# Performance work log

Measured on AMD Instinct MI355X. Metric: run time of the kernel, lower is better.

Reference implementation:

```python
import jax, jax.numpy as jnp
import numpy as np

D_IN = 1024
D_OUT = 1024
B = 4
S = 2048


def setup_inputs() -> dict:
    key = jax.random.key(0)
    kx, kq, kk, kv = jax.random.split(key, 4)
    x = jax.random.normal(kx, (B, S, D_IN), dtype=jnp.float32)
    # Linear weights stored as [d_in, d_out] so projection is x @ W
    sc = 1.0 / np.sqrt(D_IN)
    Wq = jax.random.normal(kq, (D_IN, D_OUT), dtype=jnp.float32) * sc
    Wk = jax.random.normal(kk, (D_IN, D_OUT), dtype=jnp.float32) * sc
    Wv = jax.random.normal(kv, (D_IN, D_OUT), dtype=jnp.float32) * sc
    return {"x": x, "Wq": Wq, "Wk": Wk, "Wv": Wv}


def reference(x, Wq, Wk, Wv):
    # q, k, v: [b, s, d_out]
    q = jnp.einsum("bsd,de->bse", x, Wq)
    k = jnp.einsum("bsd,de->bse", x, Wk)
    v = jnp.einsum("bsd,de->bse", x, Wv)
    s = q.shape[1]
    # raw scores [b, s, s]
    scores = jnp.einsum("bqd,bkd->bqk", q, k)
    # causal mask: disallow key j > query i (see notes re: original mask bug)
    causal = jnp.triu(jnp.ones((s, s), dtype=bool), k=1)
    scores = jnp.where(causal[None, :, :], -jnp.inf, scores)
    scale = 1.0 / jnp.sqrt(jnp.asarray(k.shape[-1], dtype=scores.dtype))
    att_weights = jax.nn.softmax(scores * scale, axis=-1)
    # dropout p=0.0 -> identity
    att_output = jnp.einsum("bqk,bkd->bqd", att_weights, v)
    return att_output, att_weights
```

## Files before the change

### kernel.cpp

```cpp
#include <hip/hip_runtime.h>
#include <stdint.h>

#define DIM 1024
#define SEQ 2048
#define NB 4

typedef unsigned short u16;
typedef __bf16 bf16x8 __attribute__((ext_vector_type(8)));
typedef float floatx4 __attribute__((ext_vector_type(4)));

__device__ __forceinline__ u16 f32_to_bf16(float f) {
  union { float f; unsigned u; } v; v.f = f;
  unsigned r = v.u + 0x7FFFu + ((v.u >> 16) & 1u);
  return (u16)(r >> 16);
}

__device__ __forceinline__ void async16(const void* g, void* l) {
  __builtin_amdgcn_global_load_lds(
      (__attribute__((address_space(1))) unsigned int*)g,
      (__attribute__((address_space(3))) unsigned int*)l, 16, 0, 0);
}

__global__ __launch_bounds__(256) void k_prep(const float* __restrict__ x,
                                              const float* __restrict__ Wq,
                                              const float* __restrict__ Wk,
                                              const float* __restrict__ Wv,
                                              u16* __restrict__ xb,
                                              u16* __restrict__ wt) {
  __shared__ u16 tile[32][33];
  const int bid = blockIdx.x;
  const int tid = threadIdx.x;
  if (bid < 4096) {
    int i = bid * 256 + tid;
    float4 a = ((const float4*)x)[i * 2];
    float4 b = ((const float4*)x)[i * 2 + 1];
    ushort4 o0, o1;
    o0.x = f32_to_bf16(a.x); o0.y = f32_to_bf16(a.y);
    o0.z = f32_to_bf16(a.z); o0.w = f32_to_bf16(a.w);
    o1.x = f32_to_bf16(b.x); o1.y = f32_to_bf16(b.y);
    o1.z = f32_to_bf16(b.z); o1.w = f32_to_bf16(b.w);
    ((ushort4*)xb)[i * 2] = o0;
    ((ushort4*)xb)[i * 2 + 1] = o1;
  } else {
    int t = bid - 4096;
    int z = t >> 10;
    int ti = t & 1023;
    int c0 = (ti & 31) * 32, r0 = (ti >> 5) * 32;
    const float* src = (z == 0) ? Wq : (z == 1) ? Wk : Wv;
    u16* d = wt + (size_t)z * DIM * DIM;
    int tx = tid & 31, ty = tid >> 5;
    #pragma unroll
    for (int dy = 0; dy < 32; dy += 8)
      tile[ty + dy][tx] = f32_to_bf16(src[(size_t)(r0 + ty + dy) * DIM + c0 + tx]);
    __syncthreads();
    #pragma unroll
    for (int dy = 0; dy < 32; dy += 8)
      d[(size_t)(c0 + ty + dy) * DIM + r0 + tx] = tile[tx][ty + dy];
  }
}


#define STG(PG, STBASE, SLOT, H, I, KT)                                        \
  async16((PG) + (size_t)((H) * 128 + (I) * 64) * DIM + (KT) * 64,             \
          (STBASE) + (SLOT) * 16384 + (H) * 8192 + (I) * 4096)

#define PHASE(SLOT, KS, MH, RDB, STAGE, SYNC)                                  \
  {                                                                            \
    const int go_ = (KS) ? ga1 : ga0;                                          \
    const u16* pa_ = aRd + (SLOT) * 16384;                                     \
    if (RDB) {                                                                 \
      const u16* pb_ = bRd + (SLOT) * 16384;                                   \
      _Pragma("unroll") for (int n = 0; n < 4; ++n)                            \
          bfr[n] = *(const bf16x8*)(pb_ + n * 1024 + go_);                     \
    }                                                                          \
    _Pragma("unroll") for (int m = 0; m < 4; ++m)                              \
        af[m] = *(const bf16x8*)(pa_ + ((MH) * 4 + m) * 1024 + go_);           \
    STAGE                                                                      \
    __builtin_amdgcn_s_barrier();                                              \
    asm volatile("s_waitcnt lgkmcnt(0)" ::: "memory");                         \
    __builtin_amdgcn_sched_barrier(0);                                         \
    __builtin_amdgcn_s_setprio(1);                                             \
    _Pragma("unroll") for (int m = 0; m < 4; ++m)                              \
        _Pragma("unroll") for (int n = 0; n < 4; ++n)                          \
            acc[(MH) * 4 + m][n] = __builtin_amdgcn_mfma_f32_16x16x32_bf16(    \
                af[m], bfr[n], acc[(MH) * 4 + m][n], 0, 0, 0);                 \
    __builtin_amdgcn_s_setprio(0);                                             \
    SYNC                                                                       \
    __builtin_amdgcn_s_barrier();                                              \
  }

__global__ __launch_bounds__(512) void k_proj8(const u16* __restrict__ xb,
                                               const u16* __restrict__ wt,
                                               u16* __restrict__ qk,
                                               u16* __restrict__ vT) {
  __shared__ u16 lds[65536];
  const int wg = ((blockIdx.x & 7) * 48) + (blockIdx.x >> 3);
  const int tid = threadIdx.x;
  const int lane = tid & 63;
  const int wid = tid >> 6;

  const u16 *A, *Bt;
  u16* Cout;
  int ldc;
  if (wg < 256) {
    const int z = wg >> 7;
    const int r = wg & 127;
    const int mt = r >> 2, nt = r & 3;
    A = xb + (size_t)mt * 256 * DIM;
    Bt = wt + (size_t)z * DIM * DIM + (size_t)nt * 256 * DIM;
    Cout = qk + (size_t)z * (NB * SEQ * DIM) + (size_t)mt * 256 * DIM + nt * 256;
    ldc = DIM;
  } else {
    const int r = wg - 256;
    const int mt = r >> 5, nt = r & 31;
    A = wt + (size_t)2 * DIM * DIM + (size_t)mt * 256 * DIM;
    Bt = xb + (size_t)nt * 256 * DIM;
    Cout = vT + (size_t)(nt >> 3) * (DIM * SEQ) + (size_t)mt * 256 * SEQ
              + (nt & 7) * 256;
    ldc = SEQ;
  }

  const int srow = wid * 8 + (lane >> 3);
  const int gsrc = (lane & 7) ^ ((lane >> 3) & 7);
  const u16* pga = A + (size_t)srow * DIM + gsrc * 8;
  const u16* pgb = Bt + (size_t)srow * DIM + gsrc * 8;
  u16* stA = lds + wid * 512;
  u16* stB = lds + 32768 + wid * 512;

  const int wr = wid >> 2, wc = wid & 3;
  const int lrow = lane & 15, quad = lane >> 4;
  const int s = lrow & 7;
  const u16* aRd = lds + (wr * 128 + lrow) * 64;
  const u16* bRd = lds + 32768 + (wc * 64 + lrow) * 64;
  const int ga0 = (quad ^ s) << 3;
  const int ga1 = ga0 ^ 32;

  floatx4 acc[8][4] = {};
  bf16x8 af[4], bfr[4];

  STG(pga, stA, 0, 0, 0, 0); STG(pga, stA, 0, 0, 1, 0);
  STG(pga, stA, 0, 1, 0, 0); STG(pga, stA, 0, 1, 1, 0);
  STG(pgb, stB, 0, 0, 0, 0); STG(pgb, stB, 0, 0, 1, 0);
  STG(pgb, stB, 0, 1, 0, 0); STG(pgb, stB, 0, 1, 1, 0);
  STG(pgb, stB, 1, 0, 0, 1); STG(pgb, stB, 1, 0, 1, 1);
  asm volatile("s_waitcnt vmcnt(2)" ::: "memory");
  __builtin_amdgcn_s_barrier();

  const int NITER = DIM / 128;
  for (int t = 0; t < NITER; ++t) {
    const bool more = (t + 1 < NITER);
    const int kA1 = 2 * t + 1;
    const int kN = 2 * t + 2;
    const int kB1n = 2 * t + 3;

    PHASE(0, 0, 0, 1,
          { STG(pga, stA, 1, 0, 0, kA1); STG(pga, stA, 1, 0, 1, kA1); }, {})
    PHASE(0, 0, 1, 0,
          { STG(pga, stA, 1, 1, 0, kA1); STG(pga, stA, 1, 1, 1, kA1); }, {})
    PHASE(0, 1, 0, 1,
          { STG(pgb, stB, 1, 1, 0, kA1); STG(pgb, stB, 1, 1, 1, kA1); }, {})
    PHASE(0, 1, 1, 0,
          { if (more) { STG(pgb, stB, 0, 0, 0, kN); STG(pgb, stB, 0, 0, 1, kN); } },
          { if (more) asm volatile("s_waitcnt vmcnt(2)" ::: "memory");
            else      asm volatile("s_waitcnt vmcnt(0)" ::: "memory"); })
    PHASE(1, 0, 0, 1,
          { if (more) { STG(pgb, stB, 0, 1, 0, kN); STG(pgb, stB, 0, 1, 1, kN); } }, {})
    PHASE(1, 0, 1, 0,
          { if (more) { STG(pga, stA, 0, 0, 0, kN); STG(pga, stA, 0, 0, 1, kN); } }, {})
    PHASE(1, 1, 0, 1,
          { if (more) { STG(pga, stA, 0, 1, 0, kN); STG(pga, stA, 0, 1, 1, kN); } }, {})
    PHASE(1, 1, 1, 0,
          { if (more) { STG(pgb, stB, 1, 0, 0, kB1n); STG(pgb, stB, 1, 0, 1, kB1n); } },
          { if (more) asm volatile("s_waitcnt vmcnt(2)" ::: "memory"); })
  }

  asm volatile("s_waitcnt vmcnt(0)" ::: "memory");

  u16* C = Cout + (size_t)(wr * 128 + quad * 4) * ldc + wc * 64 + lrow;
  #pragma unroll
  for (int m = 0; m < 8; ++m)
    #pragma unroll
    for (int rr = 0; rr < 4; ++rr)
      #pragma unroll
      for (int n = 0; n < 4; ++n)
        C[(size_t)(m * 16 + rr) * ldc + n * 16] = f32_to_bf16(acc[m][n][rr]);
}

__device__ __forceinline__ void mfma_core128(const u16* __restrict__ A, int lda,
                                             const u16* __restrict__ Bt, int ldb,
                                             int kchunks, u16* lds,
                                             floatx4 acc[4][4]) {
  const int tid = threadIdx.x;
  const int lane = tid & 63;
  const int wid = tid >> 6;
  u16* lds_a = lds;
  u16* lds_b = lds + 16384;

  const int srow4 = lane >> 4;
  const int sgr = lane & 15;
  const int gbase = sgr ^ srow4;
  const u16* ag0 = A + (size_t)(wid * 32 + srow4) * lda + gbase * 8;
  const u16* ag1 = A + (size_t)(wid * 32 + srow4) * lda + (gbase ^ 4) * 8;
  const u16* bg0 = Bt + (size_t)(wid * 32 + srow4) * ldb + gbase * 8;
  const u16* bg1 = Bt + (size_t)(wid * 32 + srow4) * ldb + (gbase ^ 4) * 8;
  u16* la = lds_a + wid * 4096;
  u16* lb = lds_b + wid * 4096;

  const int wm = (wid >> 1) * 64, wn = (wid & 1) * 64;
  const int lrow = lane & 15, quad = lane >> 4;
  const int s = lrow & 7;
  const u16* pa = lds_a + (wm + lrow) * 128;
  const u16* pb = lds_b + (wn + lrow) * 128;

  for (int kt = 0; kt < kchunks; ++kt) {
    #pragma unroll
    for (int c = 0; c < 8; ++c) {
      const u16* sa = ((c & 1) ? ag1 : ag0) + (size_t)(c * 4) * lda;
      async16(sa, la + c * 512);
    }
    #pragma unroll
    for (int c = 0; c < 8; ++c) {
      const u16* sb = ((c & 1) ? bg1 : bg0) + (size_t)(c * 4) * ldb;
      async16(sb, lb + c * 512);
    }
    ag0 += 128; ag1 += 128; bg0 += 128; bg1 += 128;
    __syncthreads();
    #pragma unroll
    for (int ks = 0; ks < 4; ++ks) {
      const int g = (((ks << 2) | quad) ^ s) << 3;
      bf16x8 af[4], bfr[4];
      #pragma unroll
      for (int t = 0; t < 4; ++t) af[t] = *(const bf16x8*)(pa + t * 2048 + g);
      #pragma unroll
      for (int t = 0; t < 4; ++t) bfr[t] = *(const bf16x8*)(pb + t * 2048 + g);
      #pragma unroll
      for (int i = 0; i < 4; ++i)
        #pragma unroll
        for (int j = 0; j < 4; ++j)
          acc[i][j] = __builtin_amdgcn_mfma_f32_16x16x32_bf16(af[i], bfr[j],
                                                              acc[i][j], 0, 0, 0);
    }
    __syncthreads();
  }
}

__global__ __launch_bounds__(256) void k_scores(const u16* __restrict__ q,
                                                const u16* __restrict__ k,
                                                float* __restrict__ w) {
  const int id = blockIdx.x;
  const int b = id & 3;
  int t = id >> 2;
  int mt = (int)((sqrtf(8.0f * (float)t + 1.0f) - 1.0f) * 0.5f);
  while ((mt + 1) * (mt + 2) / 2 <= t) ++mt;
  while (mt * (mt + 1) / 2 > t) --mt;
  const int nt = t - mt * (mt + 1) / 2;
  __shared__ u16 lds[32768];
  floatx4 acc[4][4] = {};
  mfma_core128(q + (size_t)b * SEQ * DIM + (size_t)mt * 128 * DIM, DIM,
               k + (size_t)b * SEQ * DIM + (size_t)nt * 128 * DIM, DIM,
               DIM / 128, lds, acc);
  const int lane = threadIdx.x & 63, wid = threadIdx.x >> 6;
  const int wm = (wid >> 1) * 64, wn = (wid & 1) * 64;
  const int lrow = lane & 15, quad = lane >> 4;
  float* C = w + (size_t)b * SEQ * SEQ
               + (size_t)(mt * 128 + wm + quad * 4) * SEQ + nt * 128 + wn + lrow;
  #pragma unroll
  for (int i = 0; i < 4; ++i)
    #pragma unroll
    for (int rr = 0; rr < 4; ++rr)
      #pragma unroll
      for (int j = 0; j < 4; ++j)
        C[(size_t)(i * 16 + rr) * SEQ + j * 16] = acc[i][j][rr] * 0.03125f;
}

__global__ __launch_bounds__(256) void k_softmax(float* __restrict__ w,
                                                 u16* __restrict__ P) {
  const int r = blockIdx.x;
  const int i = r & (SEQ - 1);
  const int len = i + 1;
  const int plen4 = (((i >> 7) + 1) << 7) >> 2;
  float4* srow = (float4*)(w + (size_t)r * SEQ);
  ushort4* prow = (ushort4*)(P + (size_t)r * SEQ);
  const int tid = threadIdx.x;
  const int lane = tid & 63, wid = tid >> 6;
  __shared__ float rm[4], rs[4];

  float4 e[2];
  float mx = -1e30f;
  #pragma unroll
  for (int u = 0; u < 2; ++u) {
    int q4 = tid + u * 256;
    int j0 = q4 * 4;
    float4 v = make_float4(-1e30f, -1e30f, -1e30f, -1e30f);
    if (j0 < len) {
      v = srow[q4];
      v.x = (j0 + 0 < len) ? v.x : -1e30f;
      v.y = (j0 + 1 < len) ? v.y : -1e30f;
      v.z = (j0 + 2 < len) ? v.z : -1e30f;
      v.w = (j0 + 3 < len) ? v.w : -1e30f;
    }
    e[u] = v;
    mx = fmaxf(mx, fmaxf(fmaxf(v.x, v.y), fmaxf(v.z, v.w)));
  }
  #pragma unroll
  for (int o = 32; o >= 1; o >>= 1) mx = fmaxf(mx, __shfl_xor(mx, o, 64));
  if (lane == 0) rm[wid] = mx;
  __syncthreads();
  mx = fmaxf(fmaxf(rm[0], rm[1]), fmaxf(rm[2], rm[3]));

  float sum = 0.f;
  #pragma unroll
  for (int u = 0; u < 2; ++u) {
    e[u].x = __expf(e[u].x - mx);
    e[u].y = __expf(e[u].y - mx);
    e[u].z = __expf(e[u].z - mx);
    e[u].w = __expf(e[u].w - mx);
    sum += e[u].x + e[u].y + e[u].z + e[u].w;
  }
  #pragma unroll
  for (int o = 32; o >= 1; o >>= 1) sum += __shfl_xor(sum, o, 64);
  if (lane == 0) rs[wid] = sum;
  __syncthreads();
  sum = rs[0] + rs[1] + rs[2] + rs[3];
  const float inv = 1.0f / sum;

  #pragma unroll
  for (int u = 0; u < 2; ++u) {
    int q4 = tid + u * 256;
    int j0 = q4 * 4;
    float4 v;
    v.x = (j0 + 0 < len) ? e[u].x * inv : 0.f;
    v.y = (j0 + 1 < len) ? e[u].y * inv : 0.f;
    v.z = (j0 + 2 < len) ? e[u].z * inv : 0.f;
    v.w = (j0 + 3 < len) ? e[u].w * inv : 0.f;
    srow[q4] = v;
    if (q4 < plen4) {
      ushort4 p;
      p.x = f32_to_bf16(v.x); p.y = f32_to_bf16(v.y);
      p.z = f32_to_bf16(v.z); p.w = f32_to_bf16(v.w);
      prow[q4] = p;
    }
  }
}

__global__ __launch_bounds__(256) void k_pv(const u16* __restrict__ P,
                                            const u16* __restrict__ vT,
                                            float* __restrict__ out) {
  const int id = blockIdx.x;
  const int mt = 15 - (id >> 5);
  const int nt = (id >> 2) & 7;
  const int b = id & 3;
  __shared__ u16 lds[32768];
  floatx4 acc[4][4] = {};
  mfma_core128(P + (size_t)b * SEQ * SEQ + (size_t)mt * 128 * SEQ, SEQ,
               vT + (size_t)b * DIM * SEQ + (size_t)nt * 128 * SEQ, SEQ,
               mt + 1, lds, acc);
  const int lane = threadIdx.x & 63, wid = threadIdx.x >> 6;
  const int wm = (wid >> 1) * 64, wn = (wid & 1) * 64;
  const int lrow = lane & 15, quad = lane >> 4;
  float* C = out + (size_t)b * SEQ * DIM
                 + (size_t)(mt * 128 + wm + quad * 4) * DIM + nt * 128 + wn + lrow;
  #pragma unroll
  for (int i = 0; i < 4; ++i)
    #pragma unroll
    for (int rr = 0; rr < 4; ++rr)
      #pragma unroll
      for (int j = 0; j < 4; ++j)
        C[(size_t)(i * 16 + rr) * DIM + j * 16] = acc[i][j][rr];
}

extern "C" void kernel_launch(void* const* d_in, const int* in_sizes, int n_in,
                              void* d_out, int out_size, void* d_ws, size_t ws_size,
                              hipStream_t stream) {
  const float* x  = (const float*)d_in[0];
  const float* Wq = (const float*)d_in[1];
  const float* Wk = (const float*)d_in[2];
  const float* Wv = (const float*)d_in[3];
  float* att_out = (float*)d_out;
  float* att_w   = (float*)d_out + 8388608;

  u16* xb = (u16*)d_ws;
  u16* wt = xb + 8388608;
  u16* qk = wt + 3145728;
  u16* vT = qk + 16777216;
  u16* P  = vT + 8388608;

  k_prep<<<7168, 256, 0, stream>>>(x, Wq, Wk, Wv, xb, wt);
  k_proj8<<<384, 512, 0, stream>>>(xb, wt, qk, vT);
  k_scores<<<544, 256, 0, stream>>>(qk, qk + 8388608, att_w);
  k_softmax<<<8192, 256, 0, stream>>>(att_w, P);
  k_pv<<<512, 256, 0, stream>>>(P, vT, att_out);
}
```

Before: 269.0 us.

## Double-buffer LDS fragment registers so MFMAs overlap next phase's LDS reads

```diff
diff --git a/kernel.cpp b/kernel.cpp
--- a/kernel.cpp
+++ b/kernel.cpp
@@ -64,27 +64,38 @@
   async16((PG) + (size_t)((H) * 128 + (I) * 64) * DIM + (KT) * 64,             \
           (STBASE) + (SLOT) * 16384 + (H) * 8192 + (I) * 4096)
 
-#define PHASE(SLOT, KS, MH, RDB, STAGE, SYNC)                                  \
+#define LOADAF(AF, SLOT, KS, MH)                                               \
+  { const u16* pa_ = aRd + (SLOT) * 16384;                                     \
+    const int g_ = (KS) ? ga1 : ga0;                                           \
+    AF[0] = *(const bf16x8*)(pa_ + ((MH) * 4 + 0) * 1024 + g_);                \
+    AF[1] = *(const bf16x8*)(pa_ + ((MH) * 4 + 1) * 1024 + g_);                \
+    AF[2] = *(const bf16x8*)(pa_ + ((MH) * 4 + 2) * 1024 + g_);                \
+    AF[3] = *(const bf16x8*)(pa_ + ((MH) * 4 + 3) * 1024 + g_); }
+
+#define LOADBF(BF, SLOT, KS)                                                   \
+  { const u16* pb_ = bRd + (SLOT) * 16384;                                     \
+    const int g_ = (KS) ? ga1 : ga0;                                           \
+    BF[0] = *(const bf16x8*)(pb_ + 0 * 1024 + g_);                             \
+    BF[1] = *(const bf16x8*)(pb_ + 1 * 1024 + g_);                             \
+    BF[2] = *(const bf16x8*)(pb_ + 2 * 1024 + g_);                             \
+    BF[3] = *(const bf16x8*)(pb_ + 3 * 1024 + g_); }
+
+#define MFMA16(AFU, BFU, MH)                                                   \
+  _Pragma("unroll") for (int m_ = 0; m_ < 4; ++m_)                             \
+      _Pragma("unroll") for (int n_ = 0; n_ < 4; ++n_)                         \
+          acc[(MH) * 4 + m_][n_] = __builtin_amdgcn_mfma_f32_16x16x32_bf16(    \
+              AFU[m_], BFU[n_], acc[(MH) * 4 + m_][n_], 0, 0, 0);
+
+#define PH(AFU, BFU, MH, PRELOAD, STGS, SYNC)                                  \
   {                                                                            \
-    const int go_ = (KS) ? ga1 : ga0;                                          \
-    const u16* pa_ = aRd + (SLOT) * 16384;                                     \
-    if (RDB) {                                                                 \
-      const u16* pb_ = bRd + (SLOT) * 16384;                                   \
-      _Pragma("unroll") for (int n = 0; n < 4; ++n)                            \
-          bfr[n] = *(const bf16x8*)(pb_ + n * 1024 + go_);                     \
-    }                                                                          \
-    _Pragma("unroll") for (int m = 0; m < 4; ++m)                              \
-        af[m] = *(const bf16x8*)(pa_ + ((MH) * 4 + m) * 1024 + go_);           \
-    STAGE                                                                      \
+    PRELOAD                                                                    \
+    STGS                                                                       \
     __builtin_amdgcn_s_barrier();                                              \
+    __builtin_amdgcn_s_setprio(1);                                             \
+    MFMA16(AFU, BFU, MH);                                                      \
+    __builtin_amdgcn_s_setprio(0);                                             \
     asm volatile("s_waitcnt lgkmcnt(0)" ::: "memory");                         \
     __builtin_amdgcn_sched_barrier(0);                                         \
-    __builtin_amdgcn_s_setprio(1);                                             \
-    _Pragma("unroll") for (int m = 0; m < 4; ++m)                              \
-        _Pragma("unroll") for (int n = 0; n < 4; ++n)                          \
-            acc[(MH) * 4 + m][n] = __builtin_amdgcn_mfma_f32_16x16x32_bf16(    \
-                af[m], bfr[n], acc[(MH) * 4 + m][n], 0, 0, 0);                 \
-    __builtin_amdgcn_s_setprio(0);                                             \
     SYNC                                                                       \
     __builtin_amdgcn_s_barrier();                                              \
   }
@@ -136,15 +147,20 @@
   const int ga1 = ga0 ^ 32;
 
   floatx4 acc[8][4] = {};
-  bf16x8 af[4], bfr[4];
+  bf16x8 afA[4], afB[4], bfrP[4], bfrQ[4];
 
   STG(pga, stA, 0, 0, 0, 0); STG(pga, stA, 0, 0, 1, 0);
   STG(pga, stA, 0, 1, 0, 0); STG(pga, stA, 0, 1, 1, 0);
   STG(pgb, stB, 0, 0, 0, 0); STG(pgb, stB, 0, 0, 1, 0);
   STG(pgb, stB, 0, 1, 0, 0); STG(pgb, stB, 0, 1, 1, 0);
   STG(pgb, stB, 1, 0, 0, 1); STG(pgb, stB, 1, 0, 1, 1);
-  asm volatile("s_waitcnt vmcnt(2)" ::: "memory");
+  STG(pgb, stB, 1, 1, 0, 1); STG(pgb, stB, 1, 1, 1, 1);
+  asm volatile("s_waitcnt vmcnt(4)" ::: "memory");
   __builtin_amdgcn_s_barrier();
+  LOADAF(afA, 0, 0, 0);
+  LOADBF(bfrP, 0, 0);
+  asm volatile("s_waitcnt lgkmcnt(0)" ::: "memory");
+  __builtin_amdgcn_sched_barrier(0);
 
   const int NITER = DIM / 128;
   for (int t = 0; t < NITER; ++t) {
@@ -153,25 +169,33 @@
     const int kN = 2 * t + 2;
     const int kB1n = 2 * t + 3;
 
-    PHASE(0, 0, 0, 1,
-          { STG(pga, stA, 1, 0, 0, kA1); STG(pga, stA, 1, 0, 1, kA1); }, {})
-    PHASE(0, 0, 1, 0,
-          { STG(pga, stA, 1, 1, 0, kA1); STG(pga, stA, 1, 1, 1, kA1); }, {})
-    PHASE(0, 1, 0, 1,
-          { STG(pgb, stB, 1, 1, 0, kA1); STG(pgb, stB, 1, 1, 1, kA1); }, {})
-    PHASE(0, 1, 1, 0,
-          { if (more) { STG(pgb, stB, 0, 0, 0, kN); STG(pgb, stB, 0, 0, 1, kN); } },
-          { if (more) asm volatile("s_waitcnt vmcnt(2)" ::: "memory");
-            else      asm volatile("s_waitcnt vmcnt(0)" ::: "memory"); })
-    PHASE(1, 0, 0, 1,
-          { if (more) { STG(pgb, stB, 0, 1, 0, kN); STG(pgb, stB, 0, 1, 1, kN); } }, {})
-    PHASE(1, 0, 1, 0,
-          { if (more) { STG(pga, stA, 0, 0, 0, kN); STG(pga, stA, 0, 0, 1, kN); } }, {})
-    PHASE(1, 1, 0, 1,
-          { if (more) { STG(pga, stA, 0, 1, 0, kN); STG(pga, stA, 0, 1, 1, kN); } }, {})
-    PHASE(1, 1, 1, 0,
-          { if (more) { STG(pgb, stB, 1, 0, 0, kB1n); STG(pgb, stB, 1, 0, 1, kB1n); } },
-          { if (more) asm volatile("s_waitcnt vmcnt(2)" ::: "memory"); })
+    PH(afA, bfrP, 0,
+       LOADAF(afB, 0, 0, 1);,
+       STG(pga, stA, 1, 0, 0, kA1); STG(pga, stA, 1, 0, 1, kA1);, {})
+    PH(afB, bfrP, 1,
+       LOADAF(afA, 0, 1, 0); LOADBF(bfrQ, 0, 1);,
+       STG(pga, stA, 1, 1, 0, kA1); STG(pga, stA, 1, 1, 1, kA1);, {})
+    PH(afA, bfrQ, 0,
+       LOADAF(afB, 0, 1, 1);,
+       if (more) { STG(pgb, stB, 0, 0, 0, kN); STG(pgb, stB, 0, 0, 1, kN); },
+       if (more) { asm volatile("s_waitcnt vmcnt(2)" ::: "memory"); }
+       else      { asm volatile("s_waitcnt vmcnt(0)" ::: "memory"); })
+    PH(afB, bfrQ, 1,
+       LOADAF(afA, 1, 0, 0); LOADBF(bfrP, 1, 0);,
+       if (more) { STG(pgb, stB, 0, 1, 0, kN); STG(pgb, stB, 0, 1, 1, kN); }, {})
+    PH(afA, bfrP, 0,
+       LOADAF(afB, 1, 0, 1);,
+       if (more) { STG(pga, stA, 0, 0, 0, kN); STG(pga, stA, 0, 0, 1, kN); }, {})
+    PH(afB, bfrP, 1,
+       LOADAF(afA, 1, 1, 0); LOADBF(bfrQ, 1, 1);,
+       if (more) { STG(pga, stA, 0, 1, 0, kN); STG(pga, stA, 0, 1, 1, kN); }, {})
+    PH(afA, bfrQ, 0,
+       LOADAF(afB, 1, 1, 1);,
+       if (more) { STG(pgb, stB, 1, 0, 0, kB1n); STG(pgb, stB, 1, 0, 1, kB1n); },
+       if (more) { asm volatile("s_waitcnt vmcnt(2)" ::: "memory"); })
+    PH(afB, bfrQ, 1,
+       if (more) { LOADAF(afA, 0, 0, 0); LOADBF(bfrP, 0, 0); },
+       if (more) { STG(pgb, stB, 1, 1, 0, kB1n); STG(pgb, stB, 1, 1, 1, kB1n); }, {})
   }
 
   asm volatile("s_waitcnt vmcnt(0)" ::: "memory");
```

New measurement: 270.8 us. No clear change (+0.6%).
